# Optimization experiments

Hardware: AMD Instinct MI355X
Metric: run time of the kernel (lower is better)

The kernel has to match this reference:

```python
import jax, jax.numpy as jnp
import numpy as np

NUM_CLASS = 3
SCORE_THRESH = 0.1
NMS_THRESH = 0.25
PRE = 512    # NMS_PRE_MAXSIZE (reduced from 4096 for memory; same algorithm)
POST = 100   # NMS_POST_MAXSIZE
EPS = 1e-8


def _cross(a, b):
    return a[..., 0] * b[..., 1] - a[..., 1] * b[..., 0]


def _corners(box):
    # box: (7,) = (x, y, z, dx, dy, dz, heading) -> BEV corners (4,2), CCW
    x, y, dx, dy, r = box[0], box[1], box[3], box[4], box[6]
    c, s = jnp.cos(r), jnp.sin(r)
    lx = jnp.array([0.5, -0.5, -0.5, 0.5]) * dx
    ly = jnp.array([0.5, 0.5, -0.5, -0.5]) * dy
    return jnp.stack([x + lx * c - ly * s, y + lx * s + ly * c], axis=-1)


def _in_box(pts, box):
    # pts (P,2): point-in-rotated-rect test in the box frame
    px, py = pts[:, 0] - box[0], pts[:, 1] - box[1]
    c, s = jnp.cos(box[6]), jnp.sin(box[6])
    u = px * c + py * s
    v = -px * s + py * c
    return (jnp.abs(u) <= box[3] * 0.5 + 1e-5) & (jnp.abs(v) <= box[4] * 0.5 + 1e-5)


def _bev_inter_area(ba, bb):
    # Exact rotated-rect intersection area (same construction as the CUDA
    # iou3d kernel: inside corners + edge intersections, angle-sorted shoelace).
    ca, cb = _corners(ba), _corners(bb)
    pa, ra = ca, jnp.roll(ca, -1, 0) - ca       # edges of a
    pb, rb = cb, jnp.roll(cb, -1, 0) - cb       # edges of b
    d = _cross(ra[:, None, :], rb[None, :, :])  # (4,4)
    dsafe = jnp.where(jnp.abs(d) > EPS, d, 1.0)
    qp = pb[None, :, :] - pa[:, None, :]
    t = _cross(qp, rb[None, :, :]) / dsafe
    u = _cross(qp, ra[:, None, :]) / dsafe
    vi = (jnp.abs(d) > EPS) & (t >= 0.0) & (t <= 1.0) & (u >= 0.0) & (u <= 1.0)
    ip = pa[:, None, :] + t[..., None] * ra[:, None, :]  # (4,4,2)
    pts = jnp.concatenate([ca, cb, ip.reshape(16, 2)], 0)          # (24,2)
    val = jnp.concatenate([_in_box(ca, bb), _in_box(cb, ba), vi.reshape(16)], 0)
    cnt = val.sum()
    ctr = (pts * val[:, None]).sum(0) / jnp.maximum(cnt, 1)
    ang = jnp.where(val, jnp.arctan2(pts[:, 1] - ctr[1], pts[:, 0] - ctr[0]), 1e9)
    o = jnp.argsort(ang)
    ps, vs = pts[o], val[o]
    ps = jnp.where(vs[:, None], ps, ps[0])  # collapse invalid onto first valid pt
    area = 0.5 * jnp.abs(_cross(ps, jnp.roll(ps, -1, 0)).sum())
    return jnp.where(cnt >= 3, area, 0.0)


def _iou3d(ba, bb):
    inter = _bev_inter_area(ba, bb)
    zt = jnp.minimum(ba[2] + ba[5] * 0.5, bb[2] + bb[5] * 0.5)
    zb = jnp.maximum(ba[2] - ba[5] * 0.5, bb[2] - bb[5] * 0.5)
    i3 = inter * jnp.maximum(zt - zb, 0.0)
    va = ba[3] * ba[4] * ba[5]
    vb = bb[3] * bb[4] * bb[5]
    return i3 / jnp.maximum(va + vb - i3, EPS)


_iou_mat = jax.vmap(jax.vmap(_iou3d, (None, 0)), (0, None))


def _nms(scores, boxes):
    # scores (K,) sorted descending; greedy suppression in score order
    valid = scores >= SCORE_THRESH
    iou = _iou_mat(boxes, boxes)  # (K,K)

    def body(sup, inp):
        row, v, i = inp
        keep = v & jnp.logical_not(sup[i])
        sup = sup | (keep & (row > NMS_THRESH))
        return sup, keep

    K = scores.shape[0]
    _, keep = jax.lax.scan(body, jnp.zeros((K,), bool), (iou, valid, jnp.arange(K)))
    return keep


def _post_one(cls_logits, boxes):
    # multi_classes_nms path: cls_preds_normalized=False -> sigmoid
    scores = jax.nn.sigmoid(cls_logits)  # (N, NUM_CLASS)
    out_b, out_s, out_l = [], [], []
    for k in range(NUM_CLASS):
        s = jnp.where(scores[:, k] >= SCORE_THRESH, scores[:, k], -1.0)
        top_s, idx = jax.lax.top_k(s, PRE)
        b = boxes[idx]
        keep = _nms(top_s, b)
        ks = jnp.where(keep, top_s, -1.0)
        os_, oi = jax.lax.top_k(ks, POST)
        ov = os_ >= SCORE_THRESH
        out_b.append(jnp.where(ov[:, None], b[oi], 0.0))
        out_s.append(jnp.where(ov, os_, 0.0))
        out_l.append((k + 1) * ov.astype(jnp.int32))  # final_labels = k + 1
    return (jnp.concatenate(out_b, 0), jnp.concatenate(out_s, 0),
            jnp.concatenate(out_l, 0))


def setup_inputs() -> dict:
    key = jax.random.key(0)
    k1, k2 = jax.random.split(key)
    B, N = 2, 100000
    batch_cls_preds = jax.random.normal(k1, (B, N, NUM_CLASS), dtype=jnp.float32)
    u = jax.random.uniform(k2, (B, N, 7), dtype=jnp.float32)
    x = u[..., 0] * 70.0
    y = u[..., 1] * 80.0 - 40.0
    z = u[..., 2] * 2.0 - 1.0
    dx = u[..., 3] * 3.0 + 1.5
    dy = u[..., 4] * 1.5 + 1.2
    dz = u[..., 5] * 1.0 + 1.3
    r = u[..., 6] * 2.0 * np.pi - np.pi
    batch_box_preds = jnp.stack([x, y, z, dx, dy, dz, r], axis=-1)
    return {"batch_cls_preds": batch_cls_preds, "batch_box_preds": batch_box_preds}


def reference(batch_cls_preds, batch_box_preds):
    # returns per-batch padded (pred_boxes (B, 3*POST, 7), pred_scores, pred_labels);
    # invalid slots are zeroed (label 0 == no detection)
    return jax.vmap(_post_one)(batch_cls_preds, batch_box_preds)
```

## Files before the change

### kernel.cpp

```cpp
#include <hip/hip_runtime.h>
#include <cstdint>

#define NCLS 3
#define NPTS 100000
#define NB 2
#define PRE 512
#define POST 100
#define SCORE_TH 0.1f
#define NMS_TH 0.25
#define CAP 1024
#define NBINS 384
#define XBIN_SH 16
#define XBIN_OFF (0xBFC00000u >> XBIN_SH)
#define XMARG 2e-3f
#define NPROB (NB * NCLS)
#define CPB 4
#define NKB 25
#define HPB (NCLS * NBINS)
#define BUFREG 1024
#define BUFSZ (NKB * BUFREG)
#define NCELL 36


__device__ __forceinline__ uint32_t score_key(float x)
{
    double sd = 1.0 / (1.0 + exp(-(double)x));
    float s = (float)sd;
    if (!(s >= SCORE_TH)) s = -1.0f;
    uint32_t u = __float_as_uint(s);
    return (u & 0x80000000u) ? ~u : (u | 0x80000000u);
}

__device__ __forceinline__ int xbin(float x)
{
    uint32_t u = __float_as_uint(x);
    uint32_t key = (u & 0x80000000u) ? ~u : (u | 0x80000000u);
    int b = (int)(key >> XBIN_SH) - (int)XBIN_OFF;
    return b < 0 ? 0 : (b > NBINS - 1 ? NBINS - 1 : b);
}

__global__ __launch_bounds__(1024) void hist_stage_kernel(
    const float* __restrict__ cls, uint32_t* __restrict__ hist_part,
    uint32_t* __restrict__ blkcnt, unsigned long long* __restrict__ buf)
{
    __shared__ uint32_t lh[NCLS][NBINS];
    __shared__ uint32_t lcnt3[NCLS];
    const int tid = threadIdx.x;
    for (int t = tid; t < NCLS * NBINS; t += 1024) ((uint32_t*)lh)[t] = 0;
    if (tid < NCLS) lcnt3[tid] = 0;
    __syncthreads();

    const int b = blockIdx.x / NKB, kb = blockIdx.x % NKB;
    const float* base = cls + (size_t)b * NPTS * NCLS;
    #pragma unroll
    for (int c = 0; c < CPB; ++c) {
        int i = (kb * CPB + c) * 1024 + tid;
        if (i < NPTS) {
            const float* cp = base + (size_t)i * NCLS;
            #pragma unroll
            for (int k = 0; k < NCLS; ++k) {
                float x = cp[k];
                int bn = xbin(x);
                if (bn > 0) atomicAdd(&lh[k][bn], 1u);
                if (xbin(x + XMARG) >= 1) {
                    uint32_t slot = atomicAdd(&lcnt3[k], 1u);
                    if (slot < BUFREG)
                        buf[(size_t)(b * NCLS + k) * BUFSZ + kb * BUFREG + slot]
                            = ((unsigned long long)__float_as_uint(x) << 32)
                            | (uint32_t)i;
                }
            }
        }
    }
    __syncthreads();
    uint32_t* P = hist_part + (size_t)blockIdx.x * HPB;
    for (int t = tid; t < HPB; t += 1024)
        P[t] = lh[t / NBINS][t % NBINS];
    if (tid < NCLS) {
        uint32_t c = lcnt3[tid];
        blkcnt[(b * NKB + kb) * NCLS + tid] = c < BUFREG ? c : BUFREG;
    }
}

__global__ __launch_bounds__(1024) void cell_kernel(
    const float* __restrict__ boxes, const uint32_t* __restrict__ hist_part,
    const uint32_t* __restrict__ blkcnt,
    const unsigned long long* __restrict__ buf,
    uint32_t* __restrict__ cand_idx, float* __restrict__ cand_score,
    unsigned long long* __restrict__ mask)
{
    const int blk = blockIdx.x;
    const int p = blk / NCELL;
    const int b = p / NCLS, k = p % NCLS;
    int cc = blk % NCELL;
    int wi = 0;
    while (cc >= 8 - wi) { cc -= 8 - wi; ++wi; }
    const int wj = wi + cc;
    const int tid = threadIdx.x;
    const int lane = tid & 63;
    const int wv = tid >> 6;

    __shared__ unsigned long long skey[CAP];
    __shared__ uint32_t sbins[NBINS];
    __shared__ uint32_t sblk[NKB];
    __shared__ double geo[128][20];
    __shared__ float scx[128], scy[128];
    __shared__ float sczlo[128], sczhi[128], scrad[128];
    __shared__ uint32_t lcnt;

    for (int t = tid; t < 128 * 20; t += 1024) ((double*)geo)[t] = 0.0;
    if (tid < 128) {
        scx[tid] = 0.0f; scy[tid] = 0.0f;
        sczlo[tid] = 0.0f; sczhi[tid] = 0.0f; scrad[tid] = 0.0f;
    }
    if (wi == 0 && wj == 0 && tid < PRE) {
        cand_idx[p * PRE + tid] = 0;
        cand_score[p * PRE + tid] = -1.0f;
    }
    if (tid < NKB) sblk[tid] = blkcnt[(b * NKB + tid) * NCLS + k];
    if (tid == 0) lcnt = 0;
    if (tid < NBINS) {
        uint32_t s = 0;
        const uint32_t* base2 = hist_part + (size_t)(b * NKB) * HPB
                              + k * NBINS + tid;
        #pragma unroll 5
        for (int kb = 0; kb < NKB; ++kb)
            s += base2[(size_t)kb * HPB];
        sbins[tid] = s;
    }
    __syncthreads();

    int pb;
    {
        int pbw = -1;
        uint32_t carry = 0;
        #pragma unroll
        for (int c = 5; c >= 0; --c) {
            uint32_t v = sbins[c * 64 + lane];
            #pragma unroll
            for (int off = 1; off < 64; off <<= 1) {
                uint32_t o = __shfl_down(v, off);
                v += (lane + off < 64) ? o : 0u;
            }
            uint32_t full = v + carry;
            unsigned long long bal = __ballot(full >= PRE);
            if (pbw < 0 && bal)
                pbw = c * 64 + (63 - __clzll((long long)bal));
            carry += (uint32_t)__shfl((int)v, 0);
        }
        pb = pbw < 1 ? 1 : pbw;
    }

    for (int r = 0; r < NKB; ++r) {
        if (tid < (int)sblk[r]) {
            unsigned long long e = buf[(size_t)p * BUFSZ + r * BUFREG + tid];
            float x = __uint_as_float((uint32_t)(e >> 32));
            uint32_t i = (uint32_t)e;
            if (xbin(x + XMARG) >= pb) {
                uint32_t kk = score_key(x);
                uint32_t slot = atomicAdd(&lcnt, 1u);
                if (slot < CAP)
                    skey[slot] = ((unsigned long long)kk << 32)
                               | (uint32_t)(~i);
            }
        }
    }
    __syncthreads();
    const int cnt = (int)(lcnt < CAP ? lcnt : CAP);

    unsigned long long mykey = (tid < cnt) ? skey[tid] : 0ull;
    int rank = 0;
    if (tid < cnt)
        for (int j = 0; j < cnt; ++j)
            rank += (skey[j] > mykey) ? 1 : 0;

    if (tid < cnt) {
        uint32_t idx = ~((uint32_t)mykey);
        if (wi == 0 && wj == 0 && rank < PRE) {
            uint32_t ov = (uint32_t)(mykey >> 32);
            uint32_t ub = (ov & 0x80000000u) ? (ov ^ 0x80000000u) : ~ov;
            cand_idx[p * PRE + rank] = idx;
            cand_score[p * PRE + rank] = __uint_as_float(ub);
        }
        const int slotA = rank - wi * 64;
        const int slotB = rank - wj * 64;
        const bool inA = (slotA >= 0 && slotA < 64);
        const bool inB = (slotB >= 0 && slotB < 64);
        if (inA || inB) {
            const float* bp = boxes + ((size_t)b * NPTS + idx) * 7;
            double x = bp[0], y = bp[1], z = bp[2];
            double dx = bp[3], dy = bp[4], dz = bp[5], r = bp[6];
            double c = cos(r), s = sin(r);
            double hx = 0.5 * dx, hy = 0.5 * dy;
            double zlo = z - 0.5 * dz, zhi = z + 0.5 * dz;
            double rad = sqrt(hx * hx + hy * hy);
            double V[20];
            V[0] = x; V[1] = y; V[2] = c; V[3] = s; V[4] = hx; V[5] = hy;
            V[6] = zlo; V[7] = zhi; V[8] = dx * dy * dz; V[9] = rad;
            const double lxs[4] = { hx, -hx, -hx,  hx };
            const double lys[4] = { hy,  hy, -hy, -hy };
            #pragma unroll
            for (int m = 0; m < 4; ++m) {
                V[10 + m] = x + lxs[m] * c - lys[m] * s;
                V[14 + m] = y + lxs[m] * s + lys[m] * c;
            }
            if (inA) {
                #pragma unroll
                for (int m = 0; m < 20; ++m) geo[slotA][m] = V[m];
                scx[slotA] = (float)x; scy[slotA] = (float)y;
                sczlo[slotA] = (float)zlo; sczhi[slotA] = (float)zhi;
                scrad[slotA] = (float)rad;
            }
            if (inB) {
                #pragma unroll
                for (int m = 0; m < 20; ++m) geo[64 + slotB][m] = V[m];
                scx[64 + slotB] = (float)x; scy[64 + slotB] = (float)y;
                sczlo[64 + slotB] = (float)zlo; sczhi[64 + slotB] = (float)zhi;
                scrad[64 + slotB] = (float)rad;
            }
        }
    }
    __syncthreads();

    const int half = lane >> 5;
    const int lane31 = lane & 31;
    for (int rr = wv; rr < 64; rr += 16) {
        const int bi = wi * 64 + rr;
        const double* A = geo[rr];

        bool needPoly = false;
        {
            const int jcol = wj * 64 + lane;
            if (jcol > bi) {
                float hzf = fminf(sczhi[rr], sczhi[64 + lane])
                          - fmaxf(sczlo[rr], sczlo[64 + lane]);
                if (hzf > 0.0f) {
                    float ddxf = scx[rr] - scx[64 + lane];
                    float ddyf = scy[rr] - scy[64 + lane];
                    float rsf = scrad[rr] + scrad[64 + lane] + 0.01f;
                    if (ddxf * ddxf + ddyf * ddyf <= rsf * rsf) {
                        const double* B = geo[64 + lane];
                        double hzd = fmin(A[7], B[7]) - fmax(A[6], B[6]);
                        if (hzd > 0.0) {
                            double ddx = B[0] - A[0], ddy = B[1] - A[1];
                            double ca = A[2], sa = A[3];
                            double cb2 = B[2], sb2 = B[3];
                            double cd = fabs(ca * cb2 + sa * sb2);
                            double sd = fabs(sa * cb2 - ca * sb2);
                            double pax = fabs(ddx * ca + ddy * sa);
                            double pay = fabs(-ddx * sa + ddy * ca);
                            double pbx = fabs(ddx * cb2 + ddy * sb2);
                            double pby = fabs(-ddx * sb2 + ddy * cb2);
                            if (!(pax > A[4] + B[4] * cd + B[5] * sd) &&
                                !(pay > A[5] + B[4] * sd + B[5] * cd) &&
                                !(pbx > B[4] + A[4] * cd + A[5] * sd) &&
                                !(pby > B[5] + A[4] * sd + A[5] * cd)) {
                                double areaA = 4.0 * A[4] * A[5];
                                double areaB = 4.0 * B[4] * B[5];
                                double i3m = fmin(areaA, areaB) * hzd;
                                double den = A[8] + B[8] - i3m;
                                if (den < 1e-8) den = 1e-8;
                                needPoly = (i3m / den > (double)NMS_TH);
                            }
                        }
                    }
                }
            }
        }
        unsigned long long pmask = __ballot(needPoly);
        unsigned long long supw = 0ull;

        while (pmask) {
            int jb0 = __ffsll(pmask) - 1;
            unsigned long long pm1 = pmask & (pmask - 1ull);
            int jb1 = pm1 ? (__ffsll(pm1) - 1) : -1;
            pmask = pm1 ? (pm1 & (pm1 - 1ull)) : 0ull;
            const int jb = half ? jb1 : jb0;
            const bool act = jb >= 0;
            const double* B = geo[64 + (act ? jb : 0)];

            double PX = 0.0, PY = 0.0;
            bool valid = false;
            if (act) {
                if (lane31 < 8) {
                    const double* S = (lane31 < 4) ? A : B;
                    const double* O = (lane31 < 4) ? B : A;
                    int m = lane31 & 3;
                    PX = S[10 + m]; PY = S[14 + m];
                    double rx = PX - O[0], ry = PY - O[1];
                    double u =  rx * O[2] + ry * O[3];
                    double v = -rx * O[3] + ry * O[2];
                    valid = (fabs(u) <= O[4] + 1e-5) && (fabs(v) <= O[5] + 1e-5);
                } else if (lane31 < 24) {
                    int e = lane31 - 8, m = e >> 2, nn = e & 3;
                    double ax = A[10 + m], ay = A[14 + m];
                    double rax = A[10 + ((m + 1) & 3)] - ax;
                    double ray = A[14 + ((m + 1) & 3)] - ay;
                    double bx = B[10 + nn], by = B[14 + nn];
                    double rbx = B[10 + ((nn + 1) & 3)] - bx;
                    double rby = B[14 + ((nn + 1) & 3)] - by;
                    double d = rax * rby - ray * rbx;
                    if (fabs(d) > 1e-8) {
                        double qx = bx - ax, qy = by - ay;
                        double tt = (qx * rby - qy * rbx) / d;
                        double uu = (qx * ray - qy * rax) / d;
                        valid = (tt >= 0.0 && tt <= 1.0 && uu >= 0.0 && uu <= 1.0);
                        PX = ax + tt * rax; PY = ay + tt * ray;
                    }
                }
            }
            if (!valid) { PX = 0.0; PY = 0.0; }

            unsigned long long bal = __ballot(valid);
            int cntv = __popc((uint32_t)(bal >> (half ? 32 : 0)));
            double sx = PX, sy = PY;
            #pragma unroll
            for (int off = 16; off; off >>= 1) {
                sx += __shfl_xor(sx, off);
                sy += __shfl_xor(sy, off);
            }
            int cdiv = cntv > 0 ? cntv : 1;
            double cxc = sx / cdiv, cyc = sy / cdiv;

            double ang = valid ? atan2(PY - cyc, PX - cxc) : 1e9;
            int sidx = lane31;

            #pragma unroll
            for (int kk2 = 2; kk2 <= 32; kk2 <<= 1) {
                #pragma unroll
                for (int jj = kk2 >> 1; jj > 0; jj >>= 1) {
                    double oang = __shfl_xor(ang, jj);
                    double opx  = __shfl_xor(PX, jj);
                    double opy  = __shfl_xor(PY, jj);
                    int    oidx = __shfl_xor(sidx, jj);
                    bool iLow = (lane31 & jj) == 0;
                    bool dirUp = (lane31 & kk2) == 0;
                    bool mineFirst = (ang < oang) || (ang == oang && sidx < oidx);
                    bool keepMine = (mineFirst == (iLow == dirUp));
                    if (!keepMine) { ang = oang; PX = opx; PY = opy; sidx = oidx; }
                }
            }

            double nxp = __shfl(PX, (half << 5) | ((lane31 + 1) & 31));
            double nyp = __shfl(PY, (half << 5) | ((lane31 + 1) & 31));
            double fx  = __shfl(PX, half << 5);
            double fy  = __shfl(PY, half << 5);
            bool last = (lane31 == cntv - 1);
            double qx = last ? fx : nxp, qy = last ? fy : nyp;
            double contrib = 0.0;
            if (lane31 < cntv)
                contrib = (PX - cxc) * (qy - cyc) - (PY - cyc) * (qx - cxc);
            #pragma unroll
            for (int off = 16; off; off >>= 1)
                contrib += __shfl_xor(contrib, off);
            double inter = (cntv >= 3) ? 0.5 * fabs(contrib) : 0.0;

            if (act && lane31 == 0) {
                double zt = fmin(A[7], B[7]);
                double zb = fmax(A[6], B[6]);
                double hz = zt - zb;
                bool sup = false;
                if (hz > 0.0) {
                    double i3 = inter * hz;
                    double den = A[8] + B[8] - i3;
                    if (den < 1e-8) den = 1e-8;
                    sup = (i3 / den) > (double)NMS_TH;
                }
                if (sup) supw |= 1ull << jb;
            }
        }

        supw |= __shfl_xor(supw, 32);
        if (lane == 0)
            mask[(size_t)(p * PRE + bi) * 8 + wj] = supw;
    }
}

__global__ __launch_bounds__(256) void nms_out_kernel(
    const float* __restrict__ boxes, const uint32_t* __restrict__ cand_idx,
    const float* __restrict__ cand_score,
    const unsigned long long* __restrict__ mask, float* __restrict__ out)
{
    const int p = blockIdx.x;
    const int b = p / NCLS, k = p % NCLS;
    const int tid = threadIdx.x;

    __shared__ unsigned long long smask[PRE * 8];
    __shared__ float sscore[PRE];
    __shared__ int slist[POST];
    __shared__ int scnt;

    for (int w = tid; w < PRE * 8; w += 256)
        smask[w] = mask[(size_t)p * PRE * 8 + w];
    for (int i = tid; i < PRE; i += 256)
        sscore[i] = cand_score[p * PRE + i];
    __syncthreads();

    if (tid < 64) {
        const int ln = tid;
        unsigned long long rem = 0ull;
        #pragma unroll
        for (int w = 0; w < 8; ++w) {
            unsigned long long bw = __ballot(sscore[w * 64 + ln] >= SCORE_TH);
            if (ln == w) rem = bw;
        }
        int c = 0;
        for (;;) {
            int cv = rem ? ((ln << 6) + (__ffsll(rem) - 1)) : 4096;
            int o1 = __shfl_xor(cv, 1); cv = cv < o1 ? cv : o1;
            int o2 = __shfl_xor(cv, 2); cv = cv < o2 ? cv : o2;
            int o4 = __shfl_xor(cv, 4); cv = cv < o4 ? cv : o4;
            int i = __shfl(cv, 0);
            if (i >= 4096) break;
            if (ln == 0) slist[c] = i;
            ++c;
            if (c >= POST) break;
            unsigned long long mm = (ln < 8) ? smask[i * 8 + ln] : 0ull;
            if (ln == (i >> 6)) mm |= 1ull << (i & 63);
            rem &= ~mm;
        }
        if (ln == 0) scnt = c;
    }
    __syncthreads();

    const int cnt2 = scnt;
    for (int t2 = tid; t2 < POST; t2 += 256) {
        int row = b * (NCLS * POST) + k * POST + t2;
        float* ob = out + (size_t)row * 7;
        float* os = out + (size_t)NB * NCLS * POST * 7 + row;
        float* ol = out + (size_t)NB * NCLS * POST * 7 + (size_t)NB * NCLS * POST + row;
        if (t2 < cnt2) {
            int rr = slist[t2];
            uint32_t idx = cand_idx[p * PRE + rr];
            const float* bp = boxes + ((size_t)b * NPTS + idx) * 7;
            #pragma unroll
            for (int c7 = 0; c7 < 7; ++c7) ob[c7] = bp[c7];
            *os = sscore[rr];
            *ol = (float)(k + 1);
        } else {
            #pragma unroll
            for (int c7 = 0; c7 < 7; ++c7) ob[c7] = 0.0f;
            *os = 0.0f;
            *ol = 0.0f;
        }
    }
}

extern "C" void kernel_launch(void* const* d_in, const int* in_sizes, int n_in,
                              void* d_out, int out_size, void* d_ws, size_t ws_size,
                              hipStream_t stream)
{
    (void)in_sizes; (void)n_in; (void)out_size; (void)ws_size;
    const float* cls   = (const float*)d_in[0];
    const float* boxes = (const float*)d_in[1];
    float* out = (float*)d_out;

    char* ws = (char*)d_ws;
    uint32_t* hist_part   = (uint32_t*)(ws);
    uint32_t* blkcnt      = (uint32_t*)(ws + 230400);
    unsigned long long* buf = (unsigned long long*)(ws + 231424);
    uint32_t* cand_idx    = (uint32_t*)(ws + 1460224);
    float*    cand_score  = (float*)   (ws + 1472512);
    unsigned long long* mask = (unsigned long long*)(ws + 1484800);

    hipLaunchKernelGGL(hist_stage_kernel, dim3(NB * NKB), dim3(1024), 0,
                       stream, cls, hist_part, blkcnt, buf);
    hipLaunchKernelGGL(cell_kernel, dim3(NPROB * NCELL), dim3(1024), 0,
                       stream, boxes, hist_part, blkcnt, buf,
                       cand_idx, cand_score, mask);
    hipLaunchKernelGGL(nms_out_kernel, dim3(NPROB), dim3(256), 0, stream,
                       boxes, cand_idx, cand_score, mask, out);
}
```

Baseline: 138.1 us.

## Transpose histogram partials, pad geo smem, and parallelize candidate gather across regions

Histogram partials are now stored bin-major with the producer-block index innermost, so each reducing thread reads 25 contiguous words instead of striding by a full histogram. The shared geo array is padded from 20 to 21 doubles per row to reduce LDS bank conflicts. The candidate-buffer scan now gives each quarter of the block one region at a time with 256-wide strides, which shrinks the serial 25-iteration loop. The writes in the histogram kernel become strided in exchange, and the atomic insertion order into skey changes; that order is resolved later by the rank sort.

```diff
diff --git a/kernel.cpp b/kernel.cpp
--- a/kernel.cpp
+++ b/kernel.cpp
@@ -16,10 +16,10 @@
 #define NPROB (NB * NCLS)
 #define CPB 4
 #define NKB 25
-#define HPB (NCLS * NBINS)
 #define BUFREG 1024
 #define BUFSZ (NKB * BUFREG)
 #define NCELL 36
+#define GEOP 21
 
 
 __device__ __forceinline__ uint32_t score_key(float x)
@@ -73,9 +73,11 @@
         }
     }
     __syncthreads();
-    uint32_t* P = hist_part + (size_t)blockIdx.x * HPB;
-    for (int t = tid; t < HPB; t += 1024)
-        P[t] = lh[t / NBINS][t % NBINS];
+    for (int t = tid; t < NCLS * NBINS; t += 1024) {
+        int k = t / NBINS, bin = t % NBINS;
+        hist_part[((size_t)(b * NCLS + k) * NBINS + bin) * NKB + kb]
+            = lh[k][bin];
+    }
     if (tid < NCLS) {
         uint32_t c = lcnt3[tid];
         blkcnt[(b * NKB + kb) * NCLS + tid] = c < BUFREG ? c : BUFREG;
@@ -103,12 +105,12 @@
     __shared__ unsigned long long skey[CAP];
     __shared__ uint32_t sbins[NBINS];
     __shared__ uint32_t sblk[NKB];
-    __shared__ double geo[128][20];
+    __shared__ double geo[128][GEOP];
     __shared__ float scx[128], scy[128];
     __shared__ float sczlo[128], sczhi[128], scrad[128];
     __shared__ uint32_t lcnt;
 
-    for (int t = tid; t < 128 * 20; t += 1024) ((double*)geo)[t] = 0.0;
+    for (int t = tid; t < 128 * GEOP; t += 1024) ((double*)geo)[t] = 0.0;
     if (tid < 128) {
         scx[tid] = 0.0f; scy[tid] = 0.0f;
         sczlo[tid] = 0.0f; sczhi[tid] = 0.0f; scrad[tid] = 0.0f;
@@ -120,12 +122,12 @@
     if (tid < NKB) sblk[tid] = blkcnt[(b * NKB + tid) * NCLS + k];
     if (tid == 0) lcnt = 0;
     if (tid < NBINS) {
+        const uint32_t* bp2 = hist_part
+            + ((size_t)(b * NCLS + k) * NBINS + tid) * NKB;
         uint32_t s = 0;
-        const uint32_t* base2 = hist_part + (size_t)(b * NKB) * HPB
-                              + k * NBINS + tid;
         #pragma unroll 5
         for (int kb = 0; kb < NKB; ++kb)
-            s += base2[(size_t)kb * HPB];
+            s += bp2[kb];
         sbins[tid] = s;
     }
     __syncthreads();
@@ -151,17 +153,27 @@
         pb = pbw < 1 ? 1 : pbw;
     }
 
-    for (int r = 0; r < NKB; ++r) {
-        if (tid < (int)sblk[r]) {
-            unsigned long long e = buf[(size_t)p * BUFSZ + r * BUFREG + tid];
-            float x = __uint_as_float((uint32_t)(e >> 32));
-            uint32_t i = (uint32_t)e;
-            if (xbin(x + XMARG) >= pb) {
-                uint32_t kk = score_key(x);
-                uint32_t slot = atomicAdd(&lcnt, 1u);
-                if (slot < CAP)
-                    skey[slot] = ((unsigned long long)kk << 32)
-                               | (uint32_t)(~i);
+    {
+        const int q = tid >> 8;
+        const int slot0 = tid & 255;
+        for (int r0 = 0; r0 < NKB; r0 += 4) {
+            const int r = r0 + q;
+            if (r < NKB) {
+                const uint32_t c_r = sblk[r];
+                const unsigned long long* R =
+                    buf + (size_t)p * BUFSZ + r * BUFREG;
+                for (uint32_t t = (uint32_t)slot0; t < c_r; t += 256) {
+                    unsigned long long e = R[t];
+                    float x = __uint_as_float((uint32_t)(e >> 32));
+                    uint32_t i = (uint32_t)e;
+                    if (xbin(x + XMARG) >= pb) {
+                        uint32_t kk = score_key(x);
+                        uint32_t slot = atomicAdd(&lcnt, 1u);
+                        if (slot < CAP)
+                            skey[slot] = ((unsigned long long)kk << 32)
+                                       | (uint32_t)(~i);
+                    }
+                }
             }
         }
     }
```

After: 134.0 us. -3.0%, faster.
